# Kernel optimization log

Hardware: AMD Instinct MI355X
Metric: run time of the kernel (lower is better)

## Reference

```python
import jax, jax.numpy as jnp
import numpy as np

KV_BLOCK = 128          # KV_BLOCK_SIZE in the original
EPSILON = 1e-10         # per-KV-block epsilon added to the softmax denominator


def _flash_attn(q, k, v):
    # q, k, v: [B, H, L, D]. Math identical to the original block-tiled loop:
    # online-softmax over Tc KV blocks of size 128, where each block adds
    # EPSILON to its partial row-sum. Telescoping the recursion gives:
    #   O = (exp(S - m) @ V) / (sum_j exp(S - m) + EPS * sum_blk exp(m_blk - m))
    B, H, L, D = q.shape
    scale = jnp.asarray(1.0 / np.sqrt(D), q.dtype)
    S = jnp.einsum('bhid,bhjd->bhij', q * scale, k)          # [B,H,L,L]
    m = jnp.max(S, axis=-1, keepdims=True)                   # [B,H,L,1] global row max
    Tc = L // KV_BLOCK
    # per-KV-block row maxes, for the faithful epsilon term
    m_blk = jnp.max(S.reshape(B, H, L, Tc, KV_BLOCK), axis=-1)   # [B,H,L,Tc]
    eps_term = EPSILON * jnp.sum(jnp.exp(m_blk - m), axis=-1, keepdims=True)
    P = jnp.exp(S - m)                                       # [B,H,L,L]
    l = jnp.sum(P, axis=-1, keepdims=True) + eps_term        # [B,H,L,1]
    return jnp.einsum('bhij,bhjd->bhid', P, v) / l


def setup_inputs() -> dict:
    key = jax.random.key(0)
    kq, kk, kv = jax.random.split(key, 3)
    B, L, H, D = 2, 2048, 16, 64
    return {
        'queries': jax.random.normal(kq, (B, L, H, D), dtype=jnp.float32),
        'keys': jax.random.normal(kk, (B, L, H, D), dtype=jnp.float32),
        'values': jax.random.normal(kv, (B, L, H, D), dtype=jnp.float32),
        'attn_mask': 0,  # original mask branch is broken (missing rearrange import); mask is None
    }


def reference(queries, keys, values, attn_mask):
    # inputs are [B, L, H, D]; module permutes to [B, H, L, D]
    q = jnp.transpose(queries, (0, 2, 1, 3))
    k = jnp.transpose(keys, (0, 2, 1, 3))
    v = jnp.transpose(values, (0, 2, 1, 3))
    o = _flash_attn(q, k, v)
    return jnp.transpose(o, (0, 2, 1, 3))  # back to [B, L, H, D]
```

## Files before the change

kernel.cpp:

```cpp
#include <hip/hip_runtime.h>
#include <hip/hip_bf16.h>


#define L_    2048
#define H_    16
#define D_    64
#define HD    1024
#define QBLK  128
#define KVBLK 64
#define NQT   (L_ / QBLK)

typedef short s16x8 __attribute__((ext_vector_type(8)));
typedef short s16x4 __attribute__((ext_vector_type(4)));
typedef float f32x4 __attribute__((ext_vector_type(4)));

static __device__ __forceinline__ short f2bf(float f) {
    __hip_bfloat16 h = __float2bfloat16(f);
    return *reinterpret_cast<short*>(&h);
}

__global__ __launch_bounds__(512, 2)
void fattn_kernel(const float* __restrict__ Qg, const float* __restrict__ Kg,
                  const float* __restrict__ Vg, float* __restrict__ Og)
{
    __shared__ __align__(16) short lds_k[KVBLK * D_];
    __shared__ __align__(16) short lds_v[KVBLK * D_];
    __shared__ __align__(16) short lds_p[8][16 * KVBLK];

    const int tid  = threadIdx.x;
    const int wave = tid >> 6;
    const int lane = tid & 63;
    const int q16  = lane & 15;
    const int g    = lane >> 4;

    const int bid  = blockIdx.x;
    const int virt = (bid & 7) * 64 + (bid >> 3);
    const int bh   = virt / NQT;
    const int qt   = virt % NQT;
    const int b    = bh >> 4;
    const int h    = bh & 15;

    const size_t base = (size_t)b * L_ * HD + (size_t)h * D_;
    const float* Qp = Qg + base;
    const float* Kp = Kg + base;
    const float* Vp = Vg + base;
    float*       Op = Og + base;

    s16x8 qf[2];
    {
        const float* qrow = Qp + (size_t)(qt * QBLK + wave * 16 + q16) * HD;
        #pragma unroll
        for (int c = 0; c < 2; ++c) {
            const float4 f0 = *reinterpret_cast<const float4*>(qrow + 32 * c + 8 * g);
            const float4 f1 = *reinterpret_cast<const float4*>(qrow + 32 * c + 8 * g + 4);
            s16x8 t;
            t[0] = f2bf(f0.x * 0.125f); t[1] = f2bf(f0.y * 0.125f);
            t[2] = f2bf(f0.z * 0.125f); t[3] = f2bf(f0.w * 0.125f);
            t[4] = f2bf(f1.x * 0.125f); t[5] = f2bf(f1.y * 0.125f);
            t[6] = f2bf(f1.z * 0.125f); t[7] = f2bf(f1.w * 0.125f);
            qf[c] = t;
        }
    }

    f32x4 o[4];
    #pragma unroll
    for (int i = 0; i < 4; ++i) o[i] = (f32x4){0.f, 0.f, 0.f, 0.f};
    float m_run = -INFINITY, l_run = 0.f;

    for (int kv0 = 0; kv0 < L_; kv0 += KVBLK) {
        __syncthreads();
        if (tid < 256) {
            const int kvq = tid >> 4;
            const int d0  = (tid & 15) << 2;
            const float* vb0 = Vp + (size_t)(kv0 + kvq * 4) * HD + d0;
            const float4 r0 = *reinterpret_cast<const float4*>(vb0);
            const float4 r1 = *reinterpret_cast<const float4*>(vb0 + HD);
            const float4 r2 = *reinterpret_cast<const float4*>(vb0 + 2 * HD);
            const float4 r3 = *reinterpret_cast<const float4*>(vb0 + 3 * HD);
            const float c0[4] = {r0.x, r0.y, r0.z, r0.w};
            const float c1[4] = {r1.x, r1.y, r1.z, r1.w};
            const float c2[4] = {r2.x, r2.y, r2.z, r2.w};
            const float c3[4] = {r3.x, r3.y, r3.z, r3.w};
            const int ebase = (kvq >> 1) * 512 + (kvq & 1) * 4;
            #pragma unroll
            for (int dd = 0; dd < 4; ++dd) {
                s16x4 w;
                w[0] = f2bf(c0[dd]); w[1] = f2bf(c1[dd]);
                w[2] = f2bf(c2[dd]); w[3] = f2bf(c3[dd]);
                *reinterpret_cast<s16x4*>(&lds_v[ebase + (d0 + dd) * 8]) = w;
            }
        } else {
            const int t2  = tid - 256;
            const int row = t2 >> 2;
            const int d0  = (t2 & 3) << 4;
            const float* kr = Kp + (size_t)(kv0 + row) * HD + d0;
            const float4 f0 = *reinterpret_cast<const float4*>(kr);
            const float4 f1 = *reinterpret_cast<const float4*>(kr + 4);
            const float4 f2 = *reinterpret_cast<const float4*>(kr + 8);
            const float4 f3 = *reinterpret_cast<const float4*>(kr + 12);
            s16x8 w0, w1;
            w0[0] = f2bf(f0.x); w0[1] = f2bf(f0.y); w0[2] = f2bf(f0.z); w0[3] = f2bf(f0.w);
            w0[4] = f2bf(f1.x); w0[5] = f2bf(f1.y); w0[6] = f2bf(f1.z); w0[7] = f2bf(f1.w);
            w1[0] = f2bf(f2.x); w1[1] = f2bf(f2.y); w1[2] = f2bf(f2.z); w1[3] = f2bf(f2.w);
            w1[4] = f2bf(f3.x); w1[5] = f2bf(f3.y); w1[6] = f2bf(f3.z); w1[7] = f2bf(f3.w);
            const int swz = (row & 7) << 3;
            const int e   = row * 64 + d0;
            *reinterpret_cast<s16x8*>(&lds_k[(e    ) ^ swz]) = w0;
            *reinterpret_cast<s16x8*>(&lds_k[(e + 8) ^ swz]) = w1;
        }
        __syncthreads();

        f32x4 st[4];
        #pragma unroll
        for (int mt = 0; mt < 4; ++mt) {
            st[mt] = (f32x4){0.f, 0.f, 0.f, 0.f};
            #pragma unroll
            for (int c = 0; c < 2; ++c) {
                const int row = mt * 16 + q16;
                const int e   = (row * 64 + 32 * c + 8 * g) ^ ((row & 7) << 3);
                const s16x8 kf = *reinterpret_cast<const s16x8*>(&lds_k[e]);
                st[mt] = __builtin_amdgcn_mfma_f32_16x16x32_bf16(kf, qf[c], st[mt], 0, 0, 0);
            }
        }

        float tmax = -INFINITY;
        #pragma unroll
        for (int mt = 0; mt < 4; ++mt)
            #pragma unroll
            for (int r = 0; r < 4; ++r) tmax = fmaxf(tmax, st[mt][r]);
        tmax = fmaxf(tmax, __shfl_xor(tmax, 16));
        tmax = fmaxf(tmax, __shfl_xor(tmax, 32));
        const float m_new = fmaxf(m_run, tmax);
        const float alpha = __expf(m_run - m_new);
        float p[16];
        float psum = 0.f;
        #pragma unroll
        for (int mt = 0; mt < 4; ++mt)
            #pragma unroll
            for (int r = 0; r < 4; ++r) {
                const float e = __expf(st[mt][r] - m_new);
                p[mt * 4 + r] = e;
                psum += e;
            }
        psum += __shfl_xor(psum, 16);
        psum += __shfl_xor(psum, 32);
        l_run = l_run * alpha + psum;
        m_run = m_new;

        float alpha_o[4];
        #pragma unroll
        for (int r = 0; r < 4; ++r) alpha_o[r] = __shfl(alpha, 4 * g + r);
        #pragma unroll
        for (int n = 0; n < 4; ++n)
            #pragma unroll
            for (int r = 0; r < 4; ++r) o[n][r] *= alpha_o[r];

        {
            short* pl = lds_p[wave];
            const int pswz = (q16 & 7) << 3;
            #pragma unroll
            for (int mt = 0; mt < 4; ++mt)
                #pragma unroll
                for (int r = 0; r < 4; ++r) {
                    const int kv = mt * 16 + 4 * g + r;
                    pl[(q16 * 64 + kv) ^ pswz] = f2bf(p[mt * 4 + r]);
                }
        }
        asm volatile("s_waitcnt lgkmcnt(0)" ::: "memory");
        s16x8 pa[2];
        #pragma unroll
        for (int c = 0; c < 2; ++c) {
            const int e = (q16 * 64 + 32 * c + 8 * g) ^ ((q16 & 7) << 3);
            pa[c] = *reinterpret_cast<const s16x8*>(&lds_p[wave][e]);
        }

        #pragma unroll
        for (int c = 0; c < 2; ++c) {
            #pragma unroll
            for (int n = 0; n < 4; ++n) {
                const int d = n * 16 + q16;
                const s16x8 vb = *reinterpret_cast<const s16x8*>(
                    &lds_v[(4 * c + g) * 512 + d * 8]);
                o[n] = __builtin_amdgcn_mfma_f32_16x16x32_bf16(pa[c], vb, o[n], 0, 0, 0);
            }
        }
    }

    float linv[4];
    #pragma unroll
    for (int r = 0; r < 4; ++r) linv[r] = 1.f / __shfl(l_run, 4 * g + r);
    float* orow_base = Op + (size_t)(qt * QBLK + wave * 16) * HD;
    #pragma unroll
    for (int r = 0; r < 4; ++r) {
        float* orow = orow_base + (size_t)(4 * g + r) * HD;
        #pragma unroll
        for (int n = 0; n < 4; ++n)
            orow[n * 16 + q16] = o[n][r] * linv[r];
    }
}

extern "C" void kernel_launch(void* const* d_in, const int* in_sizes, int n_in,
                              void* d_out, int out_size, void* d_ws, size_t ws_size,
                              hipStream_t stream) {
    const float* q = (const float*)d_in[0];
    const float* k = (const float*)d_in[1];
    const float* v = (const float*)d_in[2];
    float* out = (float*)d_out;
    fattn_kernel<<<dim3(512), dim3(512), 0, stream>>>(q, k, v, out);
}
```

Measured before the change: 169.1 us.

## Double-buffer K/V tiles in LDS with register prefetch of next tile

Loads the next KV tile's K and V from global memory into registers at the start of each iteration, computes on the current LDS buffer, then converts and writes the prefetched data into the alternate LDS buffer. This removes one barrier per iteration and overlaps global load latency with MFMA and softmax work. V staging is restructured so each thread loads a column strip of 8 rows and writes one 16-byte packed vector. LDS footprint and register pressure rise, which may affect occupancy.

Result: faster. 153.2 us (-9.4%).

```diff
diff --git a/kernel.cpp b/kernel.cpp
--- a/kernel.cpp
+++ b/kernel.cpp
@@ -9,9 +9,9 @@
 #define QBLK  128
 #define KVBLK 64
 #define NQT   (L_ / QBLK)
+#define NT    (L_ / KVBLK)
 
 typedef short s16x8 __attribute__((ext_vector_type(8)));
-typedef short s16x4 __attribute__((ext_vector_type(4)));
 typedef float f32x4 __attribute__((ext_vector_type(4)));
 
 static __device__ __forceinline__ short f2bf(float f) {
@@ -23,8 +23,8 @@
 void fattn_kernel(const float* __restrict__ Qg, const float* __restrict__ Kg,
                   const float* __restrict__ Vg, float* __restrict__ Og)
 {
-    __shared__ __align__(16) short lds_k[KVBLK * D_];
-    __shared__ __align__(16) short lds_v[KVBLK * D_];
+    __shared__ __align__(16) short lds_k[2][KVBLK * D_];
+    __shared__ __align__(16) short lds_v[2][KVBLK * D_];
     __shared__ __align__(16) short lds_p[8][16 * KVBLK];
 
     const int tid  = threadIdx.x;
@@ -45,6 +45,16 @@
     const float* Kp = Kg + base;
     const float* Vp = Vg + base;
     float*       Op = Og + base;
+
+    const int vks  = tid >> 6;
+    const int vd   = tid & 63;
+    const int krow = tid >> 3;
+    const int kd0  = (tid & 7) << 3;
+    const float* vcol  = Vp + vd;
+    const float* krowp = Kp + (size_t)krow * HD + kd0;
+
+    float  vreg[8];
+    float4 kreg[2];
 
     s16x8 qf[2];
     {
@@ -67,48 +77,37 @@
     for (int i = 0; i < 4; ++i) o[i] = (f32x4){0.f, 0.f, 0.f, 0.f};
     float m_run = -INFINITY, l_run = 0.f;
 
-    for (int kv0 = 0; kv0 < L_; kv0 += KVBLK) {
+    {
+        #pragma unroll
+        for (int j = 0; j < 8; ++j)
+            vreg[j] = vcol[(size_t)(8 * vks + j) * HD];
+        kreg[0] = *reinterpret_cast<const float4*>(krowp);
+        kreg[1] = *reinterpret_cast<const float4*>(krowp + 4);
+        s16x8 wv, wk;
+        #pragma unroll
+        for (int j = 0; j < 8; ++j) wv[j] = f2bf(vreg[j]);
+        wk[0] = f2bf(kreg[0].x); wk[1] = f2bf(kreg[0].y);
+        wk[2] = f2bf(kreg[0].z); wk[3] = f2bf(kreg[0].w);
+        wk[4] = f2bf(kreg[1].x); wk[5] = f2bf(kreg[1].y);
+        wk[6] = f2bf(kreg[1].z); wk[7] = f2bf(kreg[1].w);
+        *reinterpret_cast<s16x8*>(&lds_v[0][vks * 512 + vd * 8]) = wv;
+        *reinterpret_cast<s16x8*>(&lds_k[0][(krow * 64 + kd0) ^ ((krow & 7) << 3)]) = wk;
+    }
+
+    for (int t = 0; t < NT; ++t) {
+        const int cur = t & 1;
         __syncthreads();
-        if (tid < 256) {
-            const int kvq = tid >> 4;
-            const int d0  = (tid & 15) << 2;
-            const float* vb0 = Vp + (size_t)(kv0 + kvq * 4) * HD + d0;
-            const float4 r0 = *reinterpret_cast<const float4*>(vb0);
-            const float4 r1 = *reinterpret_cast<const float4*>(vb0 + HD);
-            const float4 r2 = *reinterpret_cast<const float4*>(vb0 + 2 * HD);
-            const float4 r3 = *reinterpret_cast<const float4*>(vb0 + 3 * HD);
-            const float c0[4] = {r0.x, r0.y, r0.z, r0.w};
-            const float c1[4] = {r1.x, r1.y, r1.z, r1.w};
-            const float c2[4] = {r2.x, r2.y, r2.z, r2.w};
-            const float c3[4] = {r3.x, r3.y, r3.z, r3.w};
-            const int ebase = (kvq >> 1) * 512 + (kvq & 1) * 4;
-            #pragma unroll
-            for (int dd = 0; dd < 4; ++dd) {
-                s16x4 w;
-                w[0] = f2bf(c0[dd]); w[1] = f2bf(c1[dd]);
-                w[2] = f2bf(c2[dd]); w[3] = f2bf(c3[dd]);
-                *reinterpret_cast<s16x4*>(&lds_v[ebase + (d0 + dd) * 8]) = w;
-            }
-        } else {
-            const int t2  = tid - 256;
-            const int row = t2 >> 2;
-            const int d0  = (t2 & 3) << 4;
-            const float* kr = Kp + (size_t)(kv0 + row) * HD + d0;
-            const float4 f0 = *reinterpret_cast<const float4*>(kr);
-            const float4 f1 = *reinterpret_cast<const float4*>(kr + 4);
-            const float4 f2 = *reinterpret_cast<const float4*>(kr + 8);
-            const float4 f3 = *reinterpret_cast<const float4*>(kr + 12);
-            s16x8 w0, w1;
-            w0[0] = f2bf(f0.x); w0[1] = f2bf(f0.y); w0[2] = f2bf(f0.z); w0[3] = f2bf(f0.w);
-            w0[4] = f2bf(f1.x); w0[5] = f2bf(f1.y); w0[6] = f2bf(f1.z); w0[7] = f2bf(f1.w);
-            w1[0] = f2bf(f2.x); w1[1] = f2bf(f2.y); w1[2] = f2bf(f2.z); w1[3] = f2bf(f2.w);
-            w1[4] = f2bf(f3.x); w1[5] = f2bf(f3.y); w1[6] = f2bf(f3.z); w1[7] = f2bf(f3.w);
-            const int swz = (row & 7) << 3;
-            const int e   = row * 64 + d0;
-            *reinterpret_cast<s16x8*>(&lds_k[(e    ) ^ swz]) = w0;
-            *reinterpret_cast<s16x8*>(&lds_k[(e + 8) ^ swz]) = w1;
-        }
-        __syncthreads();
+
+        if (t + 1 < NT) {
+            const int kv0n = (t + 1) * KVBLK;
+            #pragma unroll
+            for (int j = 0; j < 8; ++j)
+                vreg[j] = vcol[(size_t)(kv0n + 8 * vks + j) * HD];
+            const float* kp = krowp + (size_t)kv0n * HD;
+            kreg[0] = *reinterpret_cast<const float4*>(kp);
+            kreg[1] = *reinterpret_cast<const float4*>(kp + 4);
+        }
+        __builtin_amdgcn_sched_barrier(0);
 
         f32x4 st[4];
         #pragma unroll
@@ -118,7 +117,7 @@
             for (int c = 0; c < 2; ++c) {
                 const int row = mt * 16 + q16;
                 const int e   = (row * 64 + 32 * c + 8 * g) ^ ((row & 7) << 3);
-                const s16x8 kf = *reinterpret_cast<const s16x8*>(&lds_k[e]);
+                const s16x8 kf = *reinterpret_cast<const s16x8*>(&lds_k[cur][e]);
                 st[mt] = __builtin_amdgcn_mfma_f32_16x16x32_bf16(kf, qf[c], st[mt], 0, 0, 0);
             }
         }
@@ -180,9 +179,23 @@
             for (int n = 0; n < 4; ++n) {
                 const int d = n * 16 + q16;
                 const s16x8 vb = *reinterpret_cast<const s16x8*>(
-                    &lds_v[(4 * c + g) * 512 + d * 8]);
+                    &lds_v[cur][(4 * c + g) * 512 + d * 8]);
                 o[n] = __builtin_amdgcn_mfma_f32_16x16x32_bf16(pa[c], vb, o[n], 0, 0, 0);
             }
+        }
+
+        __builtin_amdgcn_sched_barrier(0);
+        if (t + 1 < NT) {
+            s16x8 wv, wk;
+            #pragma unroll
+            for (int j = 0; j < 8; ++j) wv[j] = f2bf(vreg[j]);
+            wk[0] = f2bf(kreg[0].x); wk[1] = f2bf(kreg[0].y);
+            wk[2] = f2bf(kreg[0].z); wk[3] = f2bf(kreg[0].w);
+            wk[4] = f2bf(kreg[1].x); wk[5] = f2bf(kreg[1].y);
+            wk[6] = f2bf(kreg[1].z); wk[7] = f2bf(kreg[1].w);
+            *reinterpret_cast<s16x8*>(&lds_v[cur ^ 1][vks * 512 + vd * 8]) = wv;
+            *reinterpret_cast<s16x8*>(
+                &lds_k[cur ^ 1][(krow * 64 + kd0) ^ ((krow & 7) << 3)]) = wk;
         }
     }
 
```
